# Optimization experiments

Measured on AMD Instinct MI355X. Metric: run time of the kernel, lower is better.

The kernel has to match this reference:

```python
import jax, jax.numpy as jnp
import numpy as np

B, T_Q, T_C = 4, 2048, 2048
Q_DIM = C_DIM = H_DIM = OUT_DIM = 1024
N_HEADS = 16
D = H_DIM // N_HEADS


def setup_inputs() -> dict:
    key = jax.random.key(0)
    ks = jax.random.split(key, 10)
    s_q = 1.0 / np.sqrt(Q_DIM)
    s_c = 1.0 / np.sqrt(C_DIM)
    s_h = 1.0 / np.sqrt(H_DIM)
    return {
        "query": jax.random.normal(ks[0], (B, T_Q, Q_DIM), jnp.float32),
        "context": jax.random.normal(ks[1], (B, T_C, C_DIM), jnp.float32),
        "Wq": jax.random.uniform(ks[2], (Q_DIM, H_DIM), jnp.float32, -s_q, s_q),
        "bq": jax.random.uniform(ks[3], (H_DIM,), jnp.float32, -s_q, s_q),
        "Wk": jax.random.uniform(ks[4], (C_DIM, H_DIM), jnp.float32, -s_c, s_c),
        "bk": jax.random.uniform(ks[5], (H_DIM,), jnp.float32, -s_c, s_c),
        "Wv": jax.random.uniform(ks[6], (C_DIM, H_DIM), jnp.float32, -s_c, s_c),
        "bv": jax.random.uniform(ks[7], (H_DIM,), jnp.float32, -s_c, s_c),
        "Wo": jax.random.uniform(ks[8], (H_DIM, OUT_DIM), jnp.float32, -s_h, s_h),
        "bo": jax.random.uniform(ks[9], (OUT_DIM,), jnp.float32, -s_h, s_h),
    }


def reference(query, context, Wq, bq, Wk, bk, Wv, bv, Wo, bo):
    Bq, Tq, _ = query.shape
    _, Tc, _ = context.shape
    # project and split heads: [B, H, T, D]
    q = (query @ Wq + bq).reshape(Bq, Tq, N_HEADS, D).transpose(0, 2, 1, 3)
    k = (context @ Wk + bk).reshape(Bq, Tc, N_HEADS, D).transpose(0, 2, 1, 3)
    v = (context @ Wv + bv).reshape(Bq, Tc, N_HEADS, D).transpose(0, 2, 1, 3)
    scores = jnp.einsum("bhqd,bhkd->bhqk", q, k) / jnp.sqrt(jnp.float32(D))
    probs = jax.nn.softmax(scores, axis=-1)
    attn = jnp.einsum("bhqk,bhkd->bhqd", probs, v)  # dropout p=0 -> identity
    attn = attn.transpose(0, 2, 1, 3).reshape(Bq, Tq, N_HEADS * D)
    return attn @ Wo + bo
```

## Files before the change

### kernel.cpp

```cpp
#include <hip/hip_runtime.h>
#include <hip/hip_bf16.h>
#include <cstdint>

typedef __attribute__((ext_vector_type(8))) short short8;
typedef __attribute__((ext_vector_type(4))) short short4_t;
typedef __attribute__((ext_vector_type(4))) float f32x4;

#define MFMA16(a, b, c) __builtin_amdgcn_mfma_f32_16x16x32_bf16(a, b, c, 0, 0, 0)

__device__ __forceinline__ short f2b(float f) {
    union { float fp; unsigned u; } un; un.fp = f;
    unsigned r = un.u + 0x7fffu + ((un.u >> 16) & 1u);
    return (short)(r >> 16);
}

__device__ __forceinline__ unsigned pk_bf16(float a, float b) {
    unsigned r;
    asm("v_cvt_pk_bf16_f32 %0, %1, %2" : "=v"(r) : "v"(a), "v"(b));
    return r;
}

union pk8_u { unsigned u4[4]; short8 s8; };
union pk4_u { unsigned u2[2]; short4_t s4; };
union cat8_u { short4_t s4[2]; short8 s8; };

typedef const __attribute__((address_space(1))) unsigned g_as1;
typedef __attribute__((address_space(3))) unsigned l_as3;
__device__ __forceinline__ void gll16(const ushort* g, ushort* l) {
    __builtin_amdgcn_global_load_lds((g_as1*)g, (l_as3*)l, 16, 0, 0);
}

__global__ __launch_bounds__(256) void cvt_all_kernel(
    const float* __restrict__ q, const float* __restrict__ c,
    ushort* __restrict__ qb, ushort* __restrict__ cb,
    const float* __restrict__ Wq, const float* __restrict__ Wk,
    const float* __restrict__ Wv, const float* __restrict__ Wo,
    ushort* __restrict__ wt)
{
    __shared__ float Ts[64 * 65];
    const int id = blockIdx.x;
    const int tid = threadIdx.x;

    if (id < 8192) {
        const float* src = (id >= 4096) ? c : q;
        ushort* dst = (id >= 4096) ? cb : qb;
        size_t i = ((size_t)(id & 4095) * 256 + tid) * 8;
        float4 v0 = *(const float4*)&src[i];
        float4 v1 = *(const float4*)&src[i + 4];
        uint4 o;
        o.x = pk_bf16(v0.x, v0.y); o.y = pk_bf16(v0.z, v0.w);
        o.z = pk_bf16(v1.x, v1.y); o.w = pk_bf16(v1.z, v1.w);
        *(uint4*)&dst[i] = o;
        return;
    }

    const int u = id - 8192;
    const int z = u >> 8;
    const float* W = (z == 0) ? Wq : (z == 1) ? Wk : (z == 2) ? Wv : Wo;
    ushort* WT = wt + (size_t)z * (1024 * 1024);
    const int n0 = (u & 15) * 64, k0 = ((u >> 4) & 15) * 64;

#pragma unroll
    for (int rr = 0; rr < 4; ++rr) {
        int uu = tid + rr * 256;
        int r = uu >> 4, cc = (uu & 15) * 4;
        float4 v = *(const float4*)&W[(size_t)(k0 + r) * 1024 + n0 + cc];
        Ts[r * 65 + cc + 0] = v.x; Ts[r * 65 + cc + 1] = v.y;
        Ts[r * 65 + cc + 2] = v.z; Ts[r * 65 + cc + 3] = v.w;
    }
    __syncthreads();
#pragma unroll
    for (int rr = 0; rr < 4; ++rr) {
        int uu = tid + rr * 256;
        int rn = uu >> 4, ck = (uu & 15) * 4;
        pk4_u o;
        o.u2[0] = pk_bf16(Ts[(ck + 0) * 65 + rn], Ts[(ck + 1) * 65 + rn]);
        o.u2[1] = pk_bf16(Ts[(ck + 2) * 65 + rn], Ts[(ck + 3) * 65 + rn]);
        *(short4_t*)&WT[(size_t)(n0 + rn) * 1024 + k0 + ck] = o.s4;
    }
}

__global__ __launch_bounds__(256) void proj_kernel(
    const ushort* __restrict__ Qb, const ushort* __restrict__ Cb,
    const ushort* __restrict__ WTbase,
    const float* __restrict__ biasq, const float* __restrict__ biask,
    const float* __restrict__ biasv,
    ushort* __restrict__ Qw, ushort* __restrict__ Kw, ushort* __restrict__ Vtw,
    float scale)
{
    __shared__ ushort As[2][128 * 64];
    const int tid = threadIdx.x;
    const int w = tid >> 6, lane = tid & 63;
    const int ln = tid & 15, quad = (tid >> 4) & 3;
    const int wm = w >> 1, wn = w & 1;

    const int hw = blockIdx.x;
    const int lid = (hw & 7) * 192 + (hw >> 3);
    const int mode = lid >> 9;
    const int rem = lid & 511;
    const int m0 = (rem >> 3) * 128;
    const int n0 = (rem & 7) * 128;
    const ushort* Ag = (mode == 2) ? Qb : Cb;
    const ushort* BT = (mode == 2) ? WTbase : WTbase + (size_t)(1 + mode) * 1048576;

    int offA[4], lseg[4];
#pragma unroll
    for (int rr = 0; rr < 4; ++rr) {
        int idx2 = (rr * 4 + w) * 64 + lane;
        int r = idx2 >> 3, cst = idx2 & 7, csrc = cst ^ (r & 7);
        offA[rr] = (m0 + r) * 1024 + csrc * 8;
        lseg[rr] = (rr * 4 + w) * 512;
    }
    const ushort* Bp = BT + (size_t)(n0 + wn * 64 + ln) * 1024;

    f32x4 acc[4][4] = {};

#pragma unroll
    for (int rr = 0; rr < 4; ++rr)
        gll16(&Ag[(size_t)offA[rr]], &As[0][lseg[rr]]);
    __syncthreads();

    for (int kt = 0; kt < 16; ++kt) {
        const int cur = kt & 1;
        if (kt < 15) {
#pragma unroll
            for (int rr = 0; rr < 4; ++rr)
                gll16(&Ag[(size_t)(offA[rr] + (kt + 1) * 64)], &As[cur ^ 1][lseg[rr]]);
        }
        const ushort* Ac = As[cur];
#pragma unroll
        for (int ks = 0; ks < 2; ++ks) {
            short8 af[4], bfr[4];
#pragma unroll
            for (int i = 0; i < 4; ++i)
                af[i] = *(const short8*)&Ac[(wm * 64 + i * 16 + ln) * 64 +
                                            ((ks * 4 + quad) ^ (ln & 7)) * 8];
#pragma unroll
            for (int j = 0; j < 4; ++j)
                bfr[j] = *(const short8*)&Bp[(size_t)(j * 16) * 1024 +
                                             kt * 64 + (ks * 4 + quad) * 8];
#pragma unroll
            for (int i = 0; i < 4; ++i)
#pragma unroll
                for (int j = 0; j < 4; ++j)
                    acc[i][j] = MFMA16(af[i], bfr[j], acc[i][j]);
        }
        __syncthreads();
    }

    if (mode == 1) {
#pragma unroll
        for (int j = 0; j < 4; ++j) {
            int n = n0 + wn * 64 + j * 16 + ln;
            int h = n >> 6, d = n & 63;
            float bvv = biasv[n];
#pragma unroll
            for (int i = 0; i < 4; ++i) {
                int mb = m0 + wm * 64 + i * 16 + quad * 4;
                int b = mb >> 11, t = mb & 2047;
                pk4_u o;
                o.u2[0] = pk_bf16(acc[i][j][0] + bvv, acc[i][j][1] + bvv);
                o.u2[1] = pk_bf16(acc[i][j][2] + bvv, acc[i][j][3] + bvv);
                *(short4_t*)&Vtw[(((size_t)((b * 16 + h) * 64 + d)) << 11) + t] = o.s4;
            }
        }
    } else {
        ushort* Out = (mode == 2) ? Qw : Kw;
        const float* bias = (mode == 2) ? biasq : biask;
        float sc = (mode == 2) ? scale : 1.0f;
#pragma unroll
        for (int j = 0; j < 4; ++j) {
            int n = n0 + wn * 64 + j * 16 + ln;
            int h = n >> 6, d = n & 63;
            float bvv = bias[n];
#pragma unroll
            for (int i = 0; i < 4; ++i) {
                int mb = m0 + wm * 64 + i * 16 + quad * 4;
#pragma unroll
                for (int r = 0; r < 4; ++r) {
                    int m = mb + r, b = m >> 11, t = m & 2047;
                    Out[(((size_t)(b * 16 + h) * 2048 + t) << 6) + d] =
                        (ushort)f2b((acc[i][j][r] + bvv) * sc);
                }
            }
        }
    }
}

__global__ __launch_bounds__(256) void gemm_o_kernel(
    const ushort* __restrict__ Ag, const ushort* __restrict__ BT,
    const float* __restrict__ bias, float* __restrict__ Out)
{
    __shared__ ushort As[2][128 * 64];
    const int tid = threadIdx.x;
    const int w = tid >> 6, lane = tid & 63;
    const int ln = tid & 15, quad = (tid >> 4) & 3;
    const int wm = w >> 1, wn = w & 1;
    const int hw = blockIdx.x;
    const int lid = (hw & 7) * 64 + (hw >> 3);
    const int m0 = (lid >> 3) * 128, n0 = (lid & 7) * 128;

    int offA[4], lseg[4];
#pragma unroll
    for (int rr = 0; rr < 4; ++rr) {
        int idx = (rr * 4 + w) * 64 + lane;
        int r = idx >> 3, cst = idx & 7, csrc = cst ^ (r & 7);
        offA[rr] = (m0 + r) * 1024 + csrc * 8;
        lseg[rr] = (rr * 4 + w) * 512;
    }
    const ushort* Bp = BT + (size_t)(n0 + wn * 64 + ln) * 1024;

    f32x4 acc[4][4] = {};

#pragma unroll
    for (int rr = 0; rr < 4; ++rr)
        gll16(&Ag[(size_t)offA[rr]], &As[0][lseg[rr]]);
    __syncthreads();

    for (int kt = 0; kt < 16; ++kt) {
        const int cur = kt & 1;
        if (kt < 15) {
#pragma unroll
            for (int rr = 0; rr < 4; ++rr)
                gll16(&Ag[(size_t)(offA[rr] + (kt + 1) * 64)], &As[cur ^ 1][lseg[rr]]);
        }
        const ushort* Ac = As[cur];
#pragma unroll
        for (int ks = 0; ks < 2; ++ks) {
            short8 af[4], bfr[4];
#pragma unroll
            for (int i = 0; i < 4; ++i)
                af[i] = *(const short8*)&Ac[(wm * 64 + i * 16 + ln) * 64 +
                                            ((ks * 4 + quad) ^ (ln & 7)) * 8];
#pragma unroll
            for (int j = 0; j < 4; ++j)
                bfr[j] = *(const short8*)&Bp[(size_t)(j * 16) * 1024 +
                                             kt * 64 + (ks * 4 + quad) * 8];
#pragma unroll
            for (int i = 0; i < 4; ++i)
#pragma unroll
                for (int j = 0; j < 4; ++j)
                    acc[i][j] = MFMA16(af[i], bfr[j], acc[i][j]);
        }
        __syncthreads();
    }

#pragma unroll
    for (int j = 0; j < 4; ++j) {
        int n = n0 + wn * 64 + j * 16 + ln;
        float bv = bias[n];
#pragma unroll
        for (int i = 0; i < 4; ++i) {
            int mb = m0 + wm * 64 + i * 16 + quad * 4;
#pragma unroll
            for (int r = 0; r < 4; ++r)
                Out[(size_t)(mb + r) * 1024 + n] = acc[i][j][r] + bv;
        }
    }
}

__global__ __launch_bounds__(256, 4) void attn_kernel(
    const ushort* __restrict__ Qw, const ushort* __restrict__ Kw,
    const ushort* __restrict__ Vtw, ushort* __restrict__ attn)
{
    __shared__ ushort Ks[2][4096];
    __shared__ ushort Vts[2][4096];

    const int tid = threadIdx.x;
    const int w = tid >> 6, lane = tid & 63;
    const int ln = tid & 15, quad = (tid >> 4) & 3;
    const int id = blockIdx.x;
    const int qt = (id >> 3) & 15;
    const int bh = (id & 7) | ((id >> 7) << 3);
    const int b = bh >> 4, h = bh & 15;

    const ushort* Qg = Qw + (size_t)bh * 131072 + (size_t)qt * 8192;
    const ushort* Kg = Kw + (size_t)bh * 131072;
    const ushort* Vg = Vtw + (size_t)bh * 131072;

    short8 bq[2][2];
#pragma unroll
    for (int qs = 0; qs < 2; ++qs)
#pragma unroll
        for (int ks = 0; ks < 2; ++ks)
            bq[qs][ks] = *(const short8*)&Qg[(w * 32 + qs * 16 + ln) * 64 + ks * 32 + quad * 8];

    int offK[2], offV[2], lseg[2];
#pragma unroll
    for (int rr = 0; rr < 2; ++rr) {
        int idx = (rr * 4 + w) * 64 + lane;
        int r = idx >> 3, cst = idx & 7, csrc = cst ^ (r & 7);
        offK[rr] = r * 64 + csrc * 8;
        offV[rr] = r * 2048 + csrc * 8;
        lseg[rr] = (rr * 4 + w) * 512;
    }

    const short8 ones8 = {(short)0x3F80, (short)0x3F80, (short)0x3F80, (short)0x3F80,
                          (short)0x3F80, (short)0x3F80, (short)0x3F80, (short)0x3F80};

    f32x4 Of[2][4] = {};
    f32x4 lac[2] = {};

#pragma unroll
    for (int rr = 0; rr < 2; ++rr) gll16(&Kg[offK[rr]], &Ks[0][lseg[rr]]);
#pragma unroll
    for (int rr = 0; rr < 2; ++rr) gll16(&Vg[offV[rr]], &Vts[0][lseg[rr]]);
    __syncthreads();

    auto body = [&](int kt, const ushort* Kc, const ushort* Vc,
                    ushort* Kn, ushort* Vn) {
        if (kt < 31) {
#pragma unroll
            for (int rr = 0; rr < 2; ++rr)
                gll16(&Kg[(kt + 1) * 4096 + offK[rr]], &Kn[lseg[rr]]);
#pragma unroll
            for (int rr = 0; rr < 2; ++rr)
                gll16(&Vg[(kt + 1) * 64 + offV[rr]], &Vn[lseg[rr]]);
        }

#pragma unroll
        for (int c = 0; c < 2; ++c) {
            short8 a0[2], a1[2];
#pragma unroll
            for (int kb = 0; kb < 2; ++kb) {
                int kv = 2 * c + kb;
                a0[kb] = *(const short8*)&Kc[(kv * 16 + ln) * 64 + (quad ^ (ln & 7)) * 8];
                a1[kb] = *(const short8*)&Kc[(kv * 16 + ln) * 64 + ((4 + quad) ^ (ln & 7)) * 8];
            }
            f32x4 s[2][2];
            __builtin_amdgcn_s_setprio(1);
#pragma unroll
            for (int kb = 0; kb < 2; ++kb)
#pragma unroll
                for (int qs = 0; qs < 2; ++qs) {
                    f32x4 t = {};
                    t = MFMA16(a0[kb], bq[qs][0], t);
                    t = MFMA16(a1[kb], bq[qs][1], t);
                    s[kb][qs] = t;
                }
            __builtin_amdgcn_s_setprio(0);

            short8 pf8[2];
#pragma unroll
            for (int qs = 0; qs < 2; ++qs) {
                pk8_u pu;
                pu.u4[0] = pk_bf16(__builtin_amdgcn_exp2f(s[0][qs][0]),
                                   __builtin_amdgcn_exp2f(s[0][qs][1]));
                pu.u4[1] = pk_bf16(__builtin_amdgcn_exp2f(s[0][qs][2]),
                                   __builtin_amdgcn_exp2f(s[0][qs][3]));
                pu.u4[2] = pk_bf16(__builtin_amdgcn_exp2f(s[1][qs][0]),
                                   __builtin_amdgcn_exp2f(s[1][qs][1]));
                pu.u4[3] = pk_bf16(__builtin_amdgcn_exp2f(s[1][qs][2]),
                                   __builtin_amdgcn_exp2f(s[1][qs][3]));
                pf8[qs] = pu.s8;
                lac[qs] = MFMA16(ones8, pu.s8, lac[qs]);
            }

            cat8_u av[4];
#pragma unroll
            for (int ds = 0; ds < 4; ++ds) {
                const ushort* vrow = &Vc[(ds * 16 + ln) * 64];
                av[ds].s4[0] = *(const short4_t*)&vrow[(((4 * c + (quad >> 1)) ^ (ln & 7)) * 8) + (quad & 1) * 4];
                av[ds].s4[1] = *(const short4_t*)&vrow[(((4 * c + 2 + (quad >> 1)) ^ (ln & 7)) * 8) + (quad & 1) * 4];
            }
            __builtin_amdgcn_s_setprio(1);
#pragma unroll
            for (int ds = 0; ds < 4; ++ds)
#pragma unroll
                for (int qs = 0; qs < 2; ++qs)
                    Of[qs][ds] = MFMA16(av[ds].s8, pf8[qs], Of[qs][ds]);
            __builtin_amdgcn_s_setprio(0);
        }

        __syncthreads();
    };

    for (int kt = 0; kt < 32; kt += 2) {
        body(kt,     Ks[0], Vts[0], Ks[1], Vts[1]);
        body(kt + 1, Ks[1], Vts[1], Ks[0], Vts[0]);
    }

#pragma unroll
    for (int qs = 0; qs < 2; ++qs) {
        float inv = __builtin_amdgcn_rcpf(lac[qs][0]);
        int t = qt * 128 + w * 32 + qs * 16 + ln;
        size_t base = ((size_t)(b * 2048 + t) << 10) + h * 64;
#pragma unroll
        for (int ds = 0; ds < 4; ++ds) {
            uint2 o;
            o.x = pk_bf16(Of[qs][ds][0] * inv, Of[qs][ds][1] * inv);
            o.y = pk_bf16(Of[qs][ds][2] * inv, Of[qs][ds][3] * inv);
            *(uint2*)&attn[base + ds * 16 + quad * 4] = o;
        }
    }
}

extern "C" void kernel_launch(void* const* d_in, const int* in_sizes, int n_in,
                              void* d_out, int out_size, void* d_ws, size_t ws_size,
                              hipStream_t stream)
{
    const float* query   = (const float*)d_in[0];
    const float* context = (const float*)d_in[1];
    const float* Wq = (const float*)d_in[2];
    const float* bq = (const float*)d_in[3];
    const float* Wk = (const float*)d_in[4];
    const float* bk = (const float*)d_in[5];
    const float* Wv = (const float*)d_in[6];
    const float* bv = (const float*)d_in[7];
    const float* Wo = (const float*)d_in[8];
    const float* bo = (const float*)d_in[9];

    char* ws = (char*)d_ws;
    ushort* WT  = (ushort*)ws;
    ushort* Qb  = (ushort*)(ws + 8388608);
    ushort* Qw  = (ushort*)(ws + 25165824);
    ushort* Kw  = (ushort*)(ws + 41943040);
    ushort* Vtw = (ushort*)(ws + 58720256);
    ushort* Aw  = Qb;
    ushort* Cb  = (ushort*)d_out;

    const float SCALE = 0.18033688011112042f;

    cvt_all_kernel<<<dim3(9216), 256, 0, stream>>>(query, context, Qb, Cb,
                                                   Wq, Wk, Wv, Wo, WT);
    proj_kernel<<<dim3(1536), 256, 0, stream>>>(Qb, Cb, WT, bq, bk, bv,
                                                Qw, Kw, Vtw, SCALE);
    attn_kernel<<<dim3(1024), 256, 0, stream>>>(Qw, Kw, Vtw, Aw);
    gemm_o_kernel<<<dim3(512), 256, 0, stream>>>(Aw, WT + 3 * 1048576, bo,
                                                 (float*)d_out);
}
```

Baseline: 349.8 us.

## Stage B operand tiles through LDS with K=32 double-buffered tiles in GEMMs

```diff
diff --git a/kernel.cpp b/kernel.cpp
--- a/kernel.cpp
+++ b/kernel.cpp
@@ -88,9 +88,10 @@
     ushort* __restrict__ Qw, ushort* __restrict__ Kw, ushort* __restrict__ Vtw,
     float scale)
 {
-    __shared__ ushort As[2][128 * 64];
+    __shared__ ushort As[2][128 * 32];
+    __shared__ ushort Bs[2][128 * 32];
     const int tid = threadIdx.x;
-    const int w = tid >> 6, lane = tid & 63;
+    const int w = tid >> 6;
     const int ln = tid & 15, quad = (tid >> 4) & 3;
     const int wm = w >> 1, wn = w & 1;
 
@@ -103,48 +104,53 @@
     const ushort* Ag = (mode == 2) ? Qb : Cb;
     const ushort* BT = (mode == 2) ? WTbase : WTbase + (size_t)(1 + mode) * 1048576;
 
-    int offA[4], lseg[4];
-#pragma unroll
-    for (int rr = 0; rr < 4; ++rr) {
-        int idx2 = (rr * 4 + w) * 64 + lane;
-        int r = idx2 >> 3, cst = idx2 & 7, csrc = cst ^ (r & 7);
-        offA[rr] = (m0 + r) * 1024 + csrc * 8;
-        lseg[rr] = (rr * 4 + w) * 512;
-    }
-    const ushort* Bp = BT + (size_t)(n0 + wn * 64 + ln) * 1024;
+    int offA[2], offB[2], lbase[2];
+#pragma unroll
+    for (int rnd = 0; rnd < 2; ++rnd) {
+        int u = rnd * 256 + tid;
+        int r = ((u >> 3) << 1) | (u & 1);
+        int c = (u >> 1) & 3;
+        int csrc = c ^ ((u >> 3) & 3);
+        offA[rnd] = (m0 + r) * 1024 + csrc * 8;
+        offB[rnd] = (n0 + r) * 1024 + csrc * 8;
+        lbase[rnd] = rnd * 2048 + w * 512;
+    }
+    const int acol = (quad ^ ((ln >> 1) & 3)) * 16 + (ln & 1) * 8;
+    const int arow = wm * 32 + (ln >> 1);
+    const int brow = wn * 32 + (ln >> 1);
 
     f32x4 acc[4][4] = {};
 
 #pragma unroll
-    for (int rr = 0; rr < 4; ++rr)
-        gll16(&Ag[(size_t)offA[rr]], &As[0][lseg[rr]]);
+    for (int rnd = 0; rnd < 2; ++rnd) {
+        gll16(&Ag[(size_t)offA[rnd]], &As[0][lbase[rnd]]);
+        gll16(&BT[(size_t)offB[rnd]], &Bs[0][lbase[rnd]]);
+    }
     __syncthreads();
 
-    for (int kt = 0; kt < 16; ++kt) {
+    for (int kt = 0; kt < 32; ++kt) {
         const int cur = kt & 1;
-        if (kt < 15) {
-#pragma unroll
-            for (int rr = 0; rr < 4; ++rr)
-                gll16(&Ag[(size_t)(offA[rr] + (kt + 1) * 64)], &As[cur ^ 1][lseg[rr]]);
+        if (kt < 31) {
+#pragma unroll
+            for (int rnd = 0; rnd < 2; ++rnd) {
+                gll16(&Ag[(size_t)(offA[rnd] + (kt + 1) * 32)], &As[cur ^ 1][lbase[rnd]]);
+                gll16(&BT[(size_t)(offB[rnd] + (kt + 1) * 32)], &Bs[cur ^ 1][lbase[rnd]]);
+            }
         }
         const ushort* Ac = As[cur];
-#pragma unroll
-        for (int ks = 0; ks < 2; ++ks) {
-            short8 af[4], bfr[4];
-#pragma unroll
-            for (int i = 0; i < 4; ++i)
-                af[i] = *(const short8*)&Ac[(wm * 64 + i * 16 + ln) * 64 +
-                                            ((ks * 4 + quad) ^ (ln & 7)) * 8];
+        const ushort* Bc = Bs[cur];
+        short8 af[4], bfr[4];
+#pragma unroll
+        for (int i = 0; i < 4; ++i)
+            af[i] = *(const short8*)&Ac[(arow + i * 8) * 64 + acol];
+#pragma unroll
+        for (int j = 0; j < 4; ++j)
+            bfr[j] = *(const short8*)&Bc[(brow + j * 8) * 64 + acol];
+#pragma unroll
+        for (int i = 0; i < 4; ++i)
 #pragma unroll
             for (int j = 0; j < 4; ++j)
-                bfr[j] = *(const short8*)&Bp[(size_t)(j * 16) * 1024 +
-                                             kt * 64 + (ks * 4 + quad) * 8];
-#pragma unroll
-            for (int i = 0; i < 4; ++i)
-#pragma unroll
-                for (int j = 0; j < 4; ++j)
-                    acc[i][j] = MFMA16(af[i], bfr[j], acc[i][j]);
-        }
+                acc[i][j] = MFMA16(af[i], bfr[j], acc[i][j]);
         __syncthreads();
     }
 
@@ -191,57 +197,63 @@
     const ushort* __restrict__ Ag, const ushort* __restrict__ BT,
     const float* __restrict__ bias, float* __restrict__ Out)
 {
-    __shared__ ushort As[2][128 * 64];
+    __shared__ ushort As[2][128 * 32];
+    __shared__ ushort Bs[2][128 * 32];
     const int tid = threadIdx.x;
-    const int w = tid >> 6, lane = tid & 63;
+    const int w = tid >> 6;
     const int ln = tid & 15, quad = (tid >> 4) & 3;
     const int wm = w >> 1, wn = w & 1;
     const int hw = blockIdx.x;
     const int lid = (hw & 7) * 64 + (hw >> 3);
     const int m0 = (lid >> 3) * 128, n0 = (lid & 7) * 128;
 
-    int offA[4], lseg[4];
-#pragma unroll
-    for (int rr = 0; rr < 4; ++rr) {
-        int idx = (rr * 4 + w) * 64 + lane;
-        int r = idx >> 3, cst = idx & 7, csrc = cst ^ (r & 7);
-        offA[rr] = (m0 + r) * 1024 + csrc * 8;
-        lseg[rr] = (rr * 4 + w) * 512;
-    }
-    const ushort* Bp = BT + (size_t)(n0 + wn * 64 + ln) * 1024;
+    int offA[2], offB[2], lbase[2];
+#pragma unroll
+    for (int rnd = 0; rnd < 2; ++rnd) {
+        int u = rnd * 256 + tid;
+        int r = ((u >> 3) << 1) | (u & 1);
+        int c = (u >> 1) & 3;
+        int csrc = c ^ ((u >> 3) & 3);
+        offA[rnd] = (m0 + r) * 1024 + csrc * 8;
+        offB[rnd] = (n0 + r) * 1024 + csrc * 8;
+        lbase[rnd] = rnd * 2048 + w * 512;
+    }
+    const int acol = (quad ^ ((ln >> 1) & 3)) * 16 + (ln & 1) * 8;
+    const int arow = wm * 32 + (ln >> 1);
+    const int brow = wn * 32 + (ln >> 1);
 
     f32x4 acc[4][4] = {};
 
 #pragma unroll
-    for (int rr = 0; rr < 4; ++rr)
-        gll16(&Ag[(size_t)offA[rr]], &As[0][lseg[rr]]);
+    for (int rnd = 0; rnd < 2; ++rnd) {
+        gll16(&Ag[(size_t)offA[rnd]], &As[0][lbase[rnd]]);
+        gll16(&BT[(size_t)offB[rnd]], &Bs[0][lbase[rnd]]);
+    }
     __syncthreads();
 
-    for (int kt = 0; kt < 16; ++kt) {
+    for (int kt = 0; kt < 32; ++kt) {
         const int cur = kt & 1;
-        if (kt < 15) {
-#pragma unroll
-            for (int rr = 0; rr < 4; ++rr)
-                gll16(&Ag[(size_t)(offA[rr] + (kt + 1) * 64)], &As[cur ^ 1][lseg[rr]]);
+        if (kt < 31) {
+#pragma unroll
+            for (int rnd = 0; rnd < 2; ++rnd) {
+                gll16(&Ag[(size_t)(offA[rnd] + (kt + 1) * 32)], &As[cur ^ 1][lbase[rnd]]);
+                gll16(&BT[(size_t)(offB[rnd] + (kt + 1) * 32)], &Bs[cur ^ 1][lbase[rnd]]);
+            }
         }
         const ushort* Ac = As[cur];
-#pragma unroll
-        for (int ks = 0; ks < 2; ++ks) {
-            short8 af[4], bfr[4];
-#pragma unroll
-            for (int i = 0; i < 4; ++i)
-                af[i] = *(const short8*)&Ac[(wm * 64 + i * 16 + ln) * 64 +
-                                            ((ks * 4 + quad) ^ (ln & 7)) * 8];
+        const ushort* Bc = Bs[cur];
+        short8 af[4], bfr[4];
+#pragma unroll
+        for (int i = 0; i < 4; ++i)
+            af[i] = *(const short8*)&Ac[(arow + i * 8) * 64 + acol];
+#pragma unroll
+        for (int j = 0; j < 4; ++j)
+            bfr[j] = *(const short8*)&Bc[(brow + j * 8) * 64 + acol];
+#pragma unroll
+        for (int i = 0; i < 4; ++i)
 #pragma unroll
             for (int j = 0; j < 4; ++j)
-                bfr[j] = *(const short8*)&Bp[(size_t)(j * 16) * 1024 +
-                                             kt * 64 + (ks * 4 + quad) * 8];
-#pragma unroll
-            for (int i = 0; i < 4; ++i)
-#pragma unroll
-                for (int j = 0; j < 4; ++j)
-                    acc[i][j] = MFMA16(af[i], bfr[j], acc[i][j]);
-        }
+                acc[i][j] = MFMA16(af[i], bfr[j], acc[i][j]);
         __syncthreads();
     }
 
```

Result: faster. 325.5 us (-7.0%).
